# Performance work log

Measured on AMD Instinct MI355X. Metric: run time of the kernel, lower is better.

Reference implementation:

```python
import jax, jax.numpy as jnp
import numpy as np

HIDDEN = 512
ATT_DIM = 128
LN_EPS = 1e-3  # keras LayerNormalization default epsilon


def setup_inputs() -> dict:
    key = jax.random.key(0)
    k1, k2, k3, k4 = jax.random.split(key, 4)
    hidden_states = jax.random.normal(k1, (64, 2048, HIDDEN), dtype=jnp.float32)
    # Glorot-uniform style init for the dense weights
    def glorot(k, shape):
        lim = np.sqrt(6.0 / (shape[0] + shape[1]))
        return jax.random.uniform(k, shape, jnp.float32, -lim, lim)
    W_a = glorot(k2, (HIDDEN, ATT_DIM))
    U_a = glorot(k3, (HIDDEN, ATT_DIM))
    v_a = glorot(k4, (ATT_DIM, 1))
    ln_gamma = jnp.ones((HIDDEN,), jnp.float32)
    ln_beta = jnp.zeros((HIDDEN,), jnp.float32)
    return {"hidden_states": hidden_states, "W_a": W_a, "U_a": U_a,
            "v_a": v_a, "ln_gamma": ln_gamma, "ln_beta": ln_beta}


def reference(hidden_states, W_a, U_a, v_a, ln_gamma, ln_beta):
    # hidden_states: (B, L, H)
    h_att = jnp.einsum('blh,ha->bla', hidden_states, W_a)        # (B, L, A)
    context = jnp.mean(hidden_states, axis=1, keepdims=True)     # (B, 1, H)
    u_att = jnp.einsum('blh,ha->bla', context, U_a)              # (B, 1, A) broadcasts
    combined = jnp.tanh(h_att + u_att)                           # (B, L, A)
    scores = jnp.einsum('bla,ao->bl', combined, v_a)             # (B, L)
    attn = jax.nn.softmax(scores, axis=-1)                       # (B, L)
    attended = jnp.einsum('blh,bl->bh', hidden_states, attn)     # (B, H)
    # LayerNormalization over last axis
    mu = jnp.mean(attended, axis=-1, keepdims=True)
    var = jnp.var(attended, axis=-1, keepdims=True)
    normed = (attended - mu) * jax.lax.rsqrt(var + LN_EPS)
    out = normed * ln_gamma + ln_beta
    return out, attn
```

## Files before the change

kernel.cpp:

```cpp
#include <hip/hip_runtime.h>
#include <hip/hip_bf16.h>

#define HIDDEN 512
#define ATT    128
#define NB     64
#define SL     2048
#define LN_EPS 1e-3f

typedef __attribute__((ext_vector_type(8))) short short8;
typedef __attribute__((ext_vector_type(4))) float f32x4;
typedef __attribute__((ext_vector_type(2))) unsigned ux2;

__device__ __forceinline__ short f2bf(float f) {
    union { float f; unsigned u; } v; v.f = f;
    unsigned r = v.u + 0x7fffu + ((v.u >> 16) & 1u);
    return (short)(r >> 16);
}
__device__ __forceinline__ unsigned pack2bf(float lo, float hi) {
    union { __hip_bfloat162 h; unsigned u; } v;
    v.h = __float22bfloat162_rn(make_float2(lo, hi));
    return v.u;
}
__device__ __forceinline__ float bflo(unsigned u) {
    union { unsigned x; float f; } v; v.x = u << 16; return v.f;
}
__device__ __forceinline__ float bfhi(unsigned u) {
    union { unsigned x; float f; } v; v.x = u & 0xffff0000u; return v.f;
}
__device__ __forceinline__ float tanh_fast(float x) {
    float cx = fminf(fmaxf(x, -15.f), 15.f);
    float e = __expf(2.f * cx);
    return (e - 1.f) * __builtin_amdgcn_rcpf(e + 1.f);
}
__device__ __forceinline__ f32x4 nt_load4(const float* p) {
    return __builtin_nontemporal_load((const f32x4*)p);
}

__global__ void p0_wt(const float* __restrict__ W, short* __restrict__ Bp) {
    int idx = blockIdx.x * 256 + threadIdx.x;
    int j = idx & 7, lane = (idx >> 3) & 63, nt = (idx >> 9) & 7, ks = idx >> 12;
    int a = nt * 16 + (lane & 15);
    int h = ks * 32 + ((lane >> 4) << 3) + j;
    Bp[idx] = f2bf(W[h * ATT + a]);
}

__launch_bounds__(256, 3)
__global__ void p1_gemm_ctx(const float* __restrict__ hidden, const short* __restrict__ Bp,
                            short* __restrict__ h_att, float* __restrict__ ctx_part) {
    __shared__ __align__(16) short As[4][2][32 * 64];

    int t = threadIdx.x;
    int wave = t >> 6, lane = t & 63, quad = lane >> 4, cb = lane & 15;
    int row0 = blockIdx.x * 128 + wave * 32;

    f32x4 acc[2][8];
    #pragma unroll
    for (int mt = 0; mt < 2; ++mt)
        #pragma unroll
        for (int nt = 0; nt < 8; ++nt)
            acc[mt][nt] = (f32x4){0.f, 0.f, 0.f, 0.f};

    int lrow = lane >> 4;
    int col4 = lane & 15;
    const float* sbase = hidden + (size_t)(row0 + lrow) * HIDDEN + col4 * 4;
    short (*my)[32 * 64] = As[wave];
    const short8* Bp8 = (const short8*)Bp + lane;

    f32x4 g[8];

    auto issue_loads = [&](int c) {
        const float* src = sbase + c * 64;
        #pragma unroll
        for (int p = 0; p < 8; ++p)
            g[p] = nt_load4(src + (size_t)p * 4 * HIDDEN);
    };

    auto pack_write = [&](int c, int buf) {
        float s[4] = {0.f, 0.f, 0.f, 0.f};
        #pragma unroll
        for (int p = 0; p < 8; ++p) {
            int row = p * 4 + lrow;
            const f32x4 f = g[p];
            s[0] += f.x; s[1] += f.y; s[2] += f.z; s[3] += f.w;
            ux2 pk;
            pk.x = pack2bf(f.x, f.y);
            pk.y = pack2bf(f.z, f.w);
            int off = row * 64 + (((col4 >> 1) ^ (row & 7)) << 3) + ((col4 & 1) << 2);
            *(ux2*)&my[buf][off] = pk;
        }
        #pragma unroll
        for (int j = 0; j < 4; ++j) {
            s[j] += __shfl_xor(s[j], 16);
            s[j] += __shfl_xor(s[j], 32);
        }
        if (lane < 16) {
            float* cp = ctx_part + (size_t)(blockIdx.x * 4 + wave) * HIDDEN + c * 64 + lane * 4;
            __builtin_nontemporal_store((f32x4){s[0], s[1], s[2], s[3]}, (f32x4*)cp);
        }
    };

    auto compute = [&](int c, int buf) {
        int swz = cb & 7;
        #pragma unroll
        for (int s2 = 0; s2 < 2; ++s2) {
            int ks = c * 2 + s2;
            short8 b8[8];
            #pragma unroll
            for (int nt = 0; nt < 8; ++nt)
                b8[nt] = Bp8[((size_t)ks * 8 + nt) * 64];
            int blk = ((s2 * 4 + quad) ^ swz) << 3;
            short8 a0 = *(const short8*)&my[buf][cb * 64 + blk];
            short8 a1 = *(const short8*)&my[buf][(cb + 16) * 64 + blk];
            #pragma unroll
            for (int nt = 0; nt < 8; ++nt) {
                acc[0][nt] = __builtin_amdgcn_mfma_f32_16x16x32_bf16(a0, b8[nt], acc[0][nt], 0, 0, 0);
                acc[1][nt] = __builtin_amdgcn_mfma_f32_16x16x32_bf16(a1, b8[nt], acc[1][nt], 0, 0, 0);
            }
        }
    };

    issue_loads(0);
    pack_write(0, 0);
    for (int c = 0; c < 8; ++c) {
        compute(c, c & 1);
        if (c < 7) {
            issue_loads(c + 1);
            pack_write(c + 1, (c + 1) & 1);
        }
    }

    ux2* hp = (ux2*)h_att;
    size_t base = (((size_t)blockIdx.x * 4 + wave) * 2) * 8 * 64 + lane;
    #pragma unroll
    for (int mt = 0; mt < 2; ++mt)
        #pragma unroll
        for (int nt = 0; nt < 8; ++nt) {
            ux2 p;
            p.x = pack2bf(acc[mt][nt][0], acc[mt][nt][1]);
            p.y = pack2bf(acc[mt][nt][2], acc[mt][nt][3]);
            __builtin_nontemporal_store(p, &hp[base + ((size_t)mt * 8 + nt) * 64]);
        }
}

__launch_bounds__(256)
__global__ void p2_uatt(const float* __restrict__ ctx_part, const float* __restrict__ U,
                        float* __restrict__ uatt) {
    int b = blockIdx.x, t = threadIdx.x;
    __shared__ float cs[HIDDEN];
    __shared__ float ds[256];
    float s0 = 0.f, s1 = 0.f;
    #pragma unroll 8
    for (int c = 0; c < 64; ++c) {
        const float* base = ctx_part + (size_t)(b * 64 + c) * HIDDEN;
        s0 += __builtin_nontemporal_load(base + t);
        s1 += __builtin_nontemporal_load(base + t + 256);
    }
    cs[t] = s0; cs[t + 256] = s1;
    __syncthreads();
    int a = t & 127, h0 = (t >> 7) * 256;
    float d = 0.f;
    #pragma unroll 8
    for (int h = 0; h < 256; ++h) d += cs[h0 + h] * U[(size_t)(h0 + h) * ATT + a];
    ds[t] = d;
    __syncthreads();
    if (t < 128) uatt[b * ATT + t] = (ds[t] + ds[t + 128]) * (1.f / SL);
}

__launch_bounds__(256)
__global__ void p3_scores(const short* __restrict__ h_att, const float* __restrict__ v_a,
                          const float* __restrict__ uatt, float* __restrict__ scores) {
    int t = threadIdx.x, bx = blockIdx.x;
    int wave = t >> 6, lane = t & 63, quad = lane >> 4, cb = lane & 15;
    int b = bx >> 4;
    int row0 = bx * 128;

    float uv[8], vv[8];
    #pragma unroll
    for (int nt = 0; nt < 8; ++nt) {
        uv[nt] = uatt[b * ATT + nt * 16 + cb];
        vv[nt] = v_a[nt * 16 + cb];
    }

    const ux2* hp = (const ux2*)h_att;
    size_t base = (((size_t)bx * 4 + wave) * 2) * 8 * 64 + lane;

    #pragma unroll
    for (int mt = 0; mt < 2; ++mt) {
        ux2 f[8];
        #pragma unroll
        for (int nt = 0; nt < 8; ++nt)
            f[nt] = __builtin_nontemporal_load(&hp[base + ((size_t)mt * 8 + nt) * 64]);
        float r[4] = {0.f, 0.f, 0.f, 0.f};
        #pragma unroll
        for (int nt = 0; nt < 8; ++nt) {
            r[0] += vv[nt] * tanh_fast(bflo(f[nt].x) + uv[nt]);
            r[1] += vv[nt] * tanh_fast(bfhi(f[nt].x) + uv[nt]);
            r[2] += vv[nt] * tanh_fast(bflo(f[nt].y) + uv[nt]);
            r[3] += vv[nt] * tanh_fast(bfhi(f[nt].y) + uv[nt]);
        }
        #pragma unroll
        for (int j = 0; j < 4; ++j) {
            r[j] += __shfl_xor(r[j], 1);
            r[j] += __shfl_xor(r[j], 2);
            r[j] += __shfl_xor(r[j], 4);
            r[j] += __shfl_xor(r[j], 8);
        }
        if (cb == 0) {
            #pragma unroll
            for (int j = 0; j < 4; ++j)
                scores[row0 + wave * 32 + mt * 16 + quad * 4 + j] = r[j];
        }
    }
}

__launch_bounds__(256)
__global__ void p4_softmax(float* __restrict__ attn) {
    int b = blockIdx.x, t = threadIdx.x;
    float* p = attn + b * SL;
    __shared__ float red[256];
    float v[8];
    float m = -1e30f;
    #pragma unroll
    for (int i = 0; i < 8; ++i) { v[i] = p[t + i * 256]; m = fmaxf(m, v[i]); }
    red[t] = m; __syncthreads();
    for (int s = 128; s > 0; s >>= 1) { if (t < s) red[t] = fmaxf(red[t], red[t + s]); __syncthreads(); }
    m = red[0]; __syncthreads();
    float sum = 0.f;
    #pragma unroll
    for (int i = 0; i < 8; ++i) { v[i] = __expf(v[i] - m); sum += v[i]; }
    red[t] = sum; __syncthreads();
    for (int s = 128; s > 0; s >>= 1) { if (t < s) red[t] += red[t + s]; __syncthreads(); }
    float inv = 1.f / red[0];
    #pragma unroll
    for (int i = 0; i < 8; ++i) p[t + i * 256] = v[i] * inv;
}

__launch_bounds__(256)
__global__ void p5_attended(const float* __restrict__ hidden, const float* __restrict__ attn,
                            float* __restrict__ att_part) {
    int b = blockIdx.y, c = blockIdx.x, t = threadIdx.x;
    __shared__ float w_s[128];
    __shared__ f32x4 red_s[128];
    if (t < 128) w_s[t] = attn[b * SL + c * 128 + t];
    __syncthreads();
    int cg = t & 127, half = t >> 7;
    const float* hp = hidden + ((size_t)b * SL + c * 128 + half * 64) * HIDDEN + cg * 4;
    f32x4 a = {0.f, 0.f, 0.f, 0.f};
    #pragma unroll 4
    for (int l = 0; l < 64; ++l) {
        float w = w_s[half * 64 + l];
        const f32x4 g = nt_load4(hp + (size_t)l * HIDDEN);
        a.x += w * g.x; a.y += w * g.y; a.z += w * g.z; a.w += w * g.w;
    }
    if (half) red_s[cg] = a;
    __syncthreads();
    if (!half) {
        f32x4 r = red_s[cg];
        a.x += r.x; a.y += r.y; a.z += r.z; a.w += r.w;
        __builtin_nontemporal_store(a, (f32x4*)(att_part + ((size_t)(c * NB + b)) * HIDDEN + cg * 4));
    }
}

__launch_bounds__(256)
__global__ void p6_ln(const float* __restrict__ att_part, const float* __restrict__ gamma,
                      const float* __restrict__ beta, float* __restrict__ out) {
    int b = blockIdx.x, t = threadIdx.x;
    float x0 = 0.f, x1 = 0.f;
    #pragma unroll
    for (int c = 0; c < 16; ++c) {
        size_t base = (size_t)(c * NB + b) * HIDDEN;
        x0 += __builtin_nontemporal_load(att_part + base + t);
        x1 += __builtin_nontemporal_load(att_part + base + t + 256);
    }
    __shared__ float rs[256], rq[256];
    rs[t] = x0 + x1; rq[t] = x0 * x0 + x1 * x1;
    __syncthreads();
    for (int s = 128; s > 0; s >>= 1) {
        if (t < s) { rs[t] += rs[t + s]; rq[t] += rq[t + s]; }
        __syncthreads();
    }
    float mean = rs[0] * (1.f / HIDDEN);
    float var = rq[0] * (1.f / HIDDEN) - mean * mean;
    float r = rsqrtf(var + LN_EPS);
    out[b * HIDDEN + t]       = (x0 - mean) * r * gamma[t] + beta[t];
    out[b * HIDDEN + t + 256] = (x1 - mean) * r * gamma[t + 256] + beta[t + 256];
}

extern "C" void kernel_launch(void* const* d_in, const int* in_sizes, int n_in,
                              void* d_out, int out_size, void* d_ws, size_t ws_size,
                              hipStream_t stream) {
    const float* hidden = (const float*)d_in[0];
    const float* W      = (const float*)d_in[1];
    const float* U      = (const float*)d_in[2];
    const float* v_a    = (const float*)d_in[3];
    const float* gamma  = (const float*)d_in[4];
    const float* beta   = (const float*)d_in[5];

    float* out  = (float*)d_out;
    float* attn = out + NB * HIDDEN;

    short* h_att    = (short*)d_ws;
    float* ctx_part = (float*)((char*)d_ws + (size_t)NB * SL * ATT * 2);
    float* att_part = ctx_part + (size_t)4096 * HIDDEN;
    float* uatt     = att_part + (size_t)16 * NB * HIDDEN;
    short* Bp       = (short*)(uatt + NB * ATT);

    p0_wt<<<256, 256, 0, stream>>>(W, Bp);
    p1_gemm_ctx<<<(NB * SL) / 128, 256, 0, stream>>>(hidden, Bp, h_att, ctx_part);
    p2_uatt<<<NB, 256, 0, stream>>>(ctx_part, U, uatt);
    p3_scores<<<(NB * SL) / 128, 256, 0, stream>>>(h_att, v_a, uatt, attn);
    p4_softmax<<<NB, 256, 0, stream>>>(attn);
    p5_attended<<<dim3(16, NB), 256, 0, stream>>>(hidden, attn, att_part);
    p6_ln<<<NB, 256, 0, stream>>>(att_part, gamma, beta, out);
}
```

Baseline: 442.9 us.

## Stage GEMM input via direct global-to-LDS loads and reverse attended-pass order for cache reuse

The GEMM kernel now copies fp32 hidden-state tiles straight into LDS with global_load_lds, using an XOR-swizzled layout. It converts them to bf16 only when reading MFMA operands, and the context partial sums are read back from LDS. This removes the register round-trip and the separate pack/write stage, at the cost of twice the LDS footprint and occupancy lowered from 3 to 2 blocks. Nontemporal loads are replaced with regular cached loads, and the attended pass walks blocks in reverse order, presumably to hit the tail of hidden_states still resident in cache from the GEMM pass.

```diff
diff --git a/kernel.cpp b/kernel.cpp
--- a/kernel.cpp
+++ b/kernel.cpp
@@ -32,8 +32,9 @@
     float e = __expf(2.f * cx);
     return (e - 1.f) * __builtin_amdgcn_rcpf(e + 1.f);
 }
-__device__ __forceinline__ f32x4 nt_load4(const float* p) {
-    return __builtin_nontemporal_load((const f32x4*)p);
+__device__ __forceinline__ void gld_lds16(const float* g, float* lds) {
+    __builtin_amdgcn_global_load_lds((const __attribute__((address_space(1))) void*)g,
+                                     (__attribute__((address_space(3))) void*)lds, 16, 0, 0);
 }
 
 __global__ void p0_wt(const float* __restrict__ W, short* __restrict__ Bp) {
@@ -44,14 +45,14 @@
     Bp[idx] = f2bf(W[h * ATT + a]);
 }
 
-__launch_bounds__(256, 3)
+__launch_bounds__(256, 2)
 __global__ void p1_gemm_ctx(const float* __restrict__ hidden, const short* __restrict__ Bp,
                             short* __restrict__ h_att, float* __restrict__ ctx_part) {
-    __shared__ __align__(16) short As[4][2][32 * 64];
+    __shared__ __align__(16) float Asf[4][2][32 * 64];
 
     int t = threadIdx.x;
     int wave = t >> 6, lane = t & 63, quad = lane >> 4, cb = lane & 15;
-    int row0 = blockIdx.x * 128 + wave * 32;
+    int row0b = blockIdx.x * 128 + wave * 32;
 
     f32x4 acc[2][8];
     #pragma unroll
@@ -60,72 +61,79 @@
         for (int nt = 0; nt < 8; ++nt)
             acc[mt][nt] = (f32x4){0.f, 0.f, 0.f, 0.f};
 
-    int lrow = lane >> 4;
-    int col4 = lane & 15;
-    const float* sbase = hidden + (size_t)(row0 + lrow) * HIDDEN + col4 * 4;
-    short (*my)[32 * 64] = As[wave];
+    const float* gsrc[8];
+    #pragma unroll
+    for (int p = 0; p < 8; ++p) {
+        int row = p * 4 + (lane >> 4);
+        int blkp = (lane & 15) ^ (row & 15);
+        gsrc[p] = hidden + (size_t)(row0b + row) * HIDDEN + blkp * 4;
+    }
+    float (*my)[32 * 64] = Asf[wave];
     const short8* Bp8 = (const short8*)Bp + lane;
 
-    f32x4 g[8];
-
-    auto issue_loads = [&](int c) {
-        const float* src = sbase + c * 64;
+    auto stage = [&](int c, int buf) {
         #pragma unroll
         for (int p = 0; p < 8; ++p)
-            g[p] = nt_load4(src + (size_t)p * 4 * HIDDEN);
+            gld_lds16(gsrc[p] + c * 64, &my[buf][p * 256]);
     };
 
-    auto pack_write = [&](int c, int buf) {
-        float s[4] = {0.f, 0.f, 0.f, 0.f};
-        #pragma unroll
-        for (int p = 0; p < 8; ++p) {
-            int row = p * 4 + lrow;
-            const f32x4 f = g[p];
-            s[0] += f.x; s[1] += f.y; s[2] += f.z; s[3] += f.w;
-            ux2 pk;
-            pk.x = pack2bf(f.x, f.y);
-            pk.y = pack2bf(f.z, f.w);
-            int off = row * 64 + (((col4 >> 1) ^ (row & 7)) << 3) + ((col4 & 1) << 2);
-            *(ux2*)&my[buf][off] = pk;
-        }
-        #pragma unroll
-        for (int j = 0; j < 4; ++j) {
-            s[j] += __shfl_xor(s[j], 16);
-            s[j] += __shfl_xor(s[j], 32);
-        }
-        if (lane < 16) {
-            float* cp = ctx_part + (size_t)(blockIdx.x * 4 + wave) * HIDDEN + c * 64 + lane * 4;
-            __builtin_nontemporal_store((f32x4){s[0], s[1], s[2], s[3]}, (f32x4*)cp);
-        }
-    };
-
-    auto compute = [&](int c, int buf) {
-        int swz = cb & 7;
+    stage(0, 0);
+
+    for (int c = 0; c < 8; ++c) {
+        int buf = c & 1;
+
+        short8 b8[2][8];
+        #pragma unroll
+        for (int s2 = 0; s2 < 2; ++s2)
+            #pragma unroll
+            for (int nt = 0; nt < 8; ++nt)
+                b8[s2][nt] = Bp8[((size_t)(c * 2 + s2) * 8 + nt) * 64];
+        __builtin_amdgcn_sched_barrier(0);
+
+        if (c < 7) stage(c + 1, buf ^ 1);
+        __builtin_amdgcn_sched_barrier(0);
+
+        asm volatile("s_waitcnt vmcnt(8)" ::: "memory");
+        __builtin_amdgcn_sched_barrier(0);
+
         #pragma unroll
         for (int s2 = 0; s2 < 2; ++s2) {
-            int ks = c * 2 + s2;
-            short8 b8[8];
-            #pragma unroll
-            for (int nt = 0; nt < 8; ++nt)
-                b8[nt] = Bp8[((size_t)ks * 8 + nt) * 64];
-            int blk = ((s2 * 4 + quad) ^ swz) << 3;
-            short8 a0 = *(const short8*)&my[buf][cb * 64 + blk];
-            short8 a1 = *(const short8*)&my[buf][(cb + 16) * 64 + blk];
+            int lb0 = (s2 * 4 + quad) * 2;
+            int o0 = (lb0 ^ cb) * 4, o1 = ((lb0 + 1) ^ cb) * 4;
+            f32x4 a0lo = *(const f32x4*)&my[buf][cb * 64 + o0];
+            f32x4 a0hi = *(const f32x4*)&my[buf][cb * 64 + o1];
+            f32x4 a1lo = *(const f32x4*)&my[buf][(cb + 16) * 64 + o0];
+            f32x4 a1hi = *(const f32x4*)&my[buf][(cb + 16) * 64 + o1];
+            union { short8 s8; unsigned u[4]; } a0p, a1p;
+            a0p.u[0] = pack2bf(a0lo.x, a0lo.y); a0p.u[1] = pack2bf(a0lo.z, a0lo.w);
+            a0p.u[2] = pack2bf(a0hi.x, a0hi.y); a0p.u[3] = pack2bf(a0hi.z, a0hi.w);
+            a1p.u[0] = pack2bf(a1lo.x, a1lo.y); a1p.u[1] = pack2bf(a1lo.z, a1lo.w);
+            a1p.u[2] = pack2bf(a1hi.x, a1hi.y); a1p.u[3] = pack2bf(a1hi.z, a1hi.w);
             #pragma unroll
             for (int nt = 0; nt < 8; ++nt) {
-                acc[0][nt] = __builtin_amdgcn_mfma_f32_16x16x32_bf16(a0, b8[nt], acc[0][nt], 0, 0, 0);
-                acc[1][nt] = __builtin_amdgcn_mfma_f32_16x16x32_bf16(a1, b8[nt], acc[1][nt], 0, 0, 0);
+                acc[0][nt] = __builtin_amdgcn_mfma_f32_16x16x32_bf16(a0p.s8, b8[s2][nt], acc[0][nt], 0, 0, 0);
+                acc[1][nt] = __builtin_amdgcn_mfma_f32_16x16x32_bf16(a1p.s8, b8[s2][nt], acc[1][nt], 0, 0, 0);
             }
         }
-    };
-
-    issue_loads(0);
-    pack_write(0, 0);
-    for (int c = 0; c < 8; ++c) {
-        compute(c, c & 1);
-        if (c < 7) {
-            issue_loads(c + 1);
-            pack_write(c + 1, (c + 1) & 1);
+
+        {
+            float s[4] = {0.f, 0.f, 0.f, 0.f};
+            #pragma unroll
+            for (int p = 0; p < 8; ++p) {
+                int row = p * 4 + (lane >> 4);
+                int phys = ((lane & 15) ^ (row & 15)) * 4;
+                f32x4 f = *(const f32x4*)&my[buf][row * 64 + phys];
+                s[0] += f.x; s[1] += f.y; s[2] += f.z; s[3] += f.w;
+            }
+            #pragma unroll
+            for (int j = 0; j < 4; ++j) {
+                s[j] += __shfl_xor(s[j], 16);
+                s[j] += __shfl_xor(s[j], 32);
+            }
+            if (lane < 16) {
+                float* cp = ctx_part + (size_t)(blockIdx.x * 4 + wave) * HIDDEN + c * 64 + lane * 4;
+                __builtin_nontemporal_store((f32x4){s[0], s[1], s[2], s[3]}, (f32x4*)cp);
+            }
         }
     }
 
@@ -152,8 +160,8 @@
     #pragma unroll 8
     for (int c = 0; c < 64; ++c) {
         const float* base = ctx_part + (size_t)(b * 64 + c) * HIDDEN;
-        s0 += __builtin_nontemporal_load(base + t);
-        s1 += __builtin_nontemporal_load(base + t + 256);
+        s0 += base[t];
+        s1 += base[t + 256];
     }
     cs[t] = s0; cs[t + 256] = s1;
     __syncthreads();
@@ -189,7 +197,7 @@
         ux2 f[8];
         #pragma unroll
         for (int nt = 0; nt < 8; ++nt)
-            f[nt] = __builtin_nontemporal_load(&hp[base + ((size_t)mt * 8 + nt) * 64]);
+            f[nt] = hp[base + ((size_t)mt * 8 + nt) * 64];
         float r[4] = {0.f, 0.f, 0.f, 0.f};
         #pragma unroll
         for (int nt = 0; nt < 8; ++nt) {
@@ -238,7 +246,7 @@
 __launch_bounds__(256)
 __global__ void p5_attended(const float* __restrict__ hidden, const float* __restrict__ attn,
                             float* __restrict__ att_part) {
-    int b = blockIdx.y, c = blockIdx.x, t = threadIdx.x;
+    int b = (NB - 1) - blockIdx.y, c = 15 - blockIdx.x, t = threadIdx.x;
     __shared__ float w_s[128];
     __shared__ f32x4 red_s[128];
     if (t < 128) w_s[t] = attn[b * SL + c * 128 + t];
@@ -249,7 +257,7 @@
     #pragma unroll 4
     for (int l = 0; l < 64; ++l) {
         float w = w_s[half * 64 + l];
-        const f32x4 g = nt_load4(hp + (size_t)l * HIDDEN);
+        const f32x4 g = *(const f32x4*)(hp + (size_t)l * HIDDEN);
         a.x += w * g.x; a.y += w * g.y; a.z += w * g.z; a.w += w * g.w;
     }
     if (half) red_s[cg] = a;
@@ -269,8 +277,8 @@
     #pragma unroll
     for (int c = 0; c < 16; ++c) {
         size_t base = (size_t)(c * NB + b) * HIDDEN;
-        x0 += __builtin_nontemporal_load(att_part + base + t);
-        x1 += __builtin_nontemporal_load(att_part + base + t + 256);
+        x0 += att_part[base + t];
+        x1 += att_part[base + t + 256];
     }
     __shared__ float rs[256], rq[256];
     rs[t] = x0 + x1; rq[t] = x0 * x0 + x1 * x1;
```

New measurement: 455.2 us. +2.8%, slower.

## Stream GEMM A tiles via global_load_lds with 16-row waves and double buffering

Applied to the files above, without the earlier changes.

The h_att GEMM now loads fp32 hidden rows straight into LDS with the global_load_lds DMA path, double-buffered with explicit vmcnt waits. Each wave handles 16 rows instead of 32, converting to bf16 at fragment read time and summing the context partials from LDS. Downstream kernels, grid sizes and the ctx_part layout are adjusted to the finer split. The aim is to cut register-staged load/pack overhead and raise occupancy, at the cost of twice as many ctx partials and less reuse of B fragments per wave.

```diff
diff --git a/kernel.cpp b/kernel.cpp
--- a/kernel.cpp
+++ b/kernel.cpp
@@ -34,6 +34,10 @@
 }
 __device__ __forceinline__ f32x4 nt_load4(const float* p) {
     return __builtin_nontemporal_load((const f32x4*)p);
+}
+__device__ __forceinline__ void gld_lds16(const float* g, float* lds) {
+    __builtin_amdgcn_global_load_lds((const __attribute__((address_space(1))) void*)g,
+                                     (__attribute__((address_space(3))) void*)lds, 16, 0, 0);
 }
 
 __global__ void p0_wt(const float* __restrict__ W, short* __restrict__ Bp) {
@@ -44,102 +48,90 @@
     Bp[idx] = f2bf(W[h * ATT + a]);
 }
 
-__launch_bounds__(256, 3)
+__launch_bounds__(256, 4)
 __global__ void p1_gemm_ctx(const float* __restrict__ hidden, const short* __restrict__ Bp,
                             short* __restrict__ h_att, float* __restrict__ ctx_part) {
-    __shared__ __align__(16) short As[4][2][32 * 64];
+    __shared__ __align__(16) float Asf[4][2][16 * 32];
 
     int t = threadIdx.x;
     int wave = t >> 6, lane = t & 63, quad = lane >> 4, cb = lane & 15;
-    int row0 = blockIdx.x * 128 + wave * 32;
-
-    f32x4 acc[2][8];
-    #pragma unroll
-    for (int mt = 0; mt < 2; ++mt)
+    int gw = blockIdx.x * 4 + wave;
+    int row0 = gw * 16;
+
+    f32x4 acc[8];
+    #pragma unroll
+    for (int nt = 0; nt < 8; ++nt) acc[nt] = (f32x4){0.f, 0.f, 0.f, 0.f};
+
+    int lr = lane >> 3;
+    int lc = lane & 7;
+    int blkp = lc ^ lr;
+    const float* g0 = hidden + (size_t)(row0 + lr) * HIDDEN + blkp * 4;
+    float (*my)[16 * 32] = Asf[wave];
+    const short8* Bp8 = (const short8*)Bp + lane;
+
+    auto stage = [&](int c, int buf) {
+        gld_lds16(g0 + c * 32,                      &my[buf][0]);
+        gld_lds16(g0 + (size_t)8 * HIDDEN + c * 32, &my[buf][8 * 32]);
+    };
+
+    stage(0, 0);
+
+    for (int c = 0; c < 16; ++c) {
+        int buf = c & 1;
+
+        short8 b8[8];
         #pragma unroll
         for (int nt = 0; nt < 8; ++nt)
-            acc[mt][nt] = (f32x4){0.f, 0.f, 0.f, 0.f};
-
-    int lrow = lane >> 4;
-    int col4 = lane & 15;
-    const float* sbase = hidden + (size_t)(row0 + lrow) * HIDDEN + col4 * 4;
-    short (*my)[32 * 64] = As[wave];
-    const short8* Bp8 = (const short8*)Bp + lane;
-
-    f32x4 g[8];
-
-    auto issue_loads = [&](int c) {
-        const float* src = sbase + c * 64;
-        #pragma unroll
-        for (int p = 0; p < 8; ++p)
-            g[p] = nt_load4(src + (size_t)p * 4 * HIDDEN);
-    };
-
-    auto pack_write = [&](int c, int buf) {
-        float s[4] = {0.f, 0.f, 0.f, 0.f};
-        #pragma unroll
-        for (int p = 0; p < 8; ++p) {
-            int row = p * 4 + lrow;
-            const f32x4 f = g[p];
-            s[0] += f.x; s[1] += f.y; s[2] += f.z; s[3] += f.w;
-            ux2 pk;
-            pk.x = pack2bf(f.x, f.y);
-            pk.y = pack2bf(f.z, f.w);
-            int off = row * 64 + (((col4 >> 1) ^ (row & 7)) << 3) + ((col4 & 1) << 2);
-            *(ux2*)&my[buf][off] = pk;
-        }
-        #pragma unroll
-        for (int j = 0; j < 4; ++j) {
-            s[j] += __shfl_xor(s[j], 16);
-            s[j] += __shfl_xor(s[j], 32);
-        }
-        if (lane < 16) {
-            float* cp = ctx_part + (size_t)(blockIdx.x * 4 + wave) * HIDDEN + c * 64 + lane * 4;
-            __builtin_nontemporal_store((f32x4){s[0], s[1], s[2], s[3]}, (f32x4*)cp);
-        }
-    };
-
-    auto compute = [&](int c, int buf) {
-        int swz = cb & 7;
-        #pragma unroll
-        for (int s2 = 0; s2 < 2; ++s2) {
-            int ks = c * 2 + s2;
-            short8 b8[8];
+            b8[nt] = Bp8[((size_t)c * 8 + nt) * 64];
+        __builtin_amdgcn_sched_barrier(0);
+
+        if (c < 15) stage(c + 1, buf ^ 1);
+        __builtin_amdgcn_sched_barrier(0);
+
+        if (c < 15) { asm volatile("s_waitcnt vmcnt(2)" ::: "memory"); }
+        else        { asm volatile("s_waitcnt vmcnt(0)" ::: "memory"); }
+        __builtin_amdgcn_sched_barrier(0);
+
+        {
+            int lb0 = quad * 2;
+            int o0 = ((lb0 ^ (cb & 7)) << 2);
+            int o1 = (((lb0 + 1) ^ (cb & 7)) << 2);
+            f32x4 alo = *(const f32x4*)&my[buf][cb * 32 + o0];
+            f32x4 ahi = *(const f32x4*)&my[buf][cb * 32 + o1];
+            union { short8 s8; unsigned u[4]; } ap;
+            ap.u[0] = pack2bf(alo.x, alo.y); ap.u[1] = pack2bf(alo.z, alo.w);
+            ap.u[2] = pack2bf(ahi.x, ahi.y); ap.u[3] = pack2bf(ahi.z, ahi.w);
             #pragma unroll
             for (int nt = 0; nt < 8; ++nt)
-                b8[nt] = Bp8[((size_t)ks * 8 + nt) * 64];
-            int blk = ((s2 * 4 + quad) ^ swz) << 3;
-            short8 a0 = *(const short8*)&my[buf][cb * 64 + blk];
-            short8 a1 = *(const short8*)&my[buf][(cb + 16) * 64 + blk];
+                acc[nt] = __builtin_amdgcn_mfma_f32_16x16x32_bf16(ap.s8, b8[nt], acc[nt], 0, 0, 0);
+        }
+
+        {
+            f32x4 f0 = *(const f32x4*)&my[buf][lr * 32 + (blkp << 2)];
+            f32x4 f1 = *(const f32x4*)&my[buf][(lr + 8) * 32 + (blkp << 2)];
+            float s[4] = { f0.x + f1.x, f0.y + f1.y, f0.z + f1.z, f0.w + f1.w };
             #pragma unroll
-            for (int nt = 0; nt < 8; ++nt) {
-                acc[0][nt] = __builtin_amdgcn_mfma_f32_16x16x32_bf16(a0, b8[nt], acc[0][nt], 0, 0, 0);
-                acc[1][nt] = __builtin_amdgcn_mfma_f32_16x16x32_bf16(a1, b8[nt], acc[1][nt], 0, 0, 0);
+            for (int j = 0; j < 4; ++j) {
+                s[j] += __shfl_xor(s[j], 8);
+                s[j] += __shfl_xor(s[j], 16);
+                s[j] += __shfl_xor(s[j], 32);
+            }
+            if (lane < 8) {
+                float* cp = ctx_part + (size_t)gw * HIDDEN + c * 32 + lane * 4;
+                __builtin_nontemporal_store((f32x4){s[0], s[1], s[2], s[3]}, (f32x4*)cp);
             }
         }
-    };
-
-    issue_loads(0);
-    pack_write(0, 0);
-    for (int c = 0; c < 8; ++c) {
-        compute(c, c & 1);
-        if (c < 7) {
-            issue_loads(c + 1);
-            pack_write(c + 1, (c + 1) & 1);
-        }
     }
 
     ux2* hp = (ux2*)h_att;
-    size_t base = (((size_t)blockIdx.x * 4 + wave) * 2) * 8 * 64 + lane;
-    #pragma unroll
-    for (int mt = 0; mt < 2; ++mt)
-        #pragma unroll
-        for (int nt = 0; nt < 8; ++nt) {
-            ux2 p;
-            p.x = pack2bf(acc[mt][nt][0], acc[mt][nt][1]);
-            p.y = pack2bf(acc[mt][nt][2], acc[mt][nt][3]);
-            __builtin_nontemporal_store(p, &hp[base + ((size_t)mt * 8 + nt) * 64]);
-        }
+    size_t base = (size_t)gw * 8 * 64 + lane;
+    #pragma unroll
+    for (int nt = 0; nt < 8; ++nt) {
+        ux2 p;
+        p.x = pack2bf(acc[nt][0], acc[nt][1]);
+        p.y = pack2bf(acc[nt][2], acc[nt][3]);
+        __builtin_nontemporal_store(p, &hp[base + (size_t)nt * 64]);
+    }
 }
 
 __launch_bounds__(256)
@@ -150,8 +142,8 @@
     __shared__ float ds[256];
     float s0 = 0.f, s1 = 0.f;
     #pragma unroll 8
-    for (int c = 0; c < 64; ++c) {
-        const float* base = ctx_part + (size_t)(b * 64 + c) * HIDDEN;
+    for (int c = 0; c < 128; ++c) {
+        const float* base = ctx_part + (size_t)(b * 128 + c) * HIDDEN;
         s0 += __builtin_nontemporal_load(base + t);
         s1 += __builtin_nontemporal_load(base + t + 256);
     }
@@ -171,8 +163,8 @@
                           const float* __restrict__ uatt, float* __restrict__ scores) {
     int t = threadIdx.x, bx = blockIdx.x;
     int wave = t >> 6, lane = t & 63, quad = lane >> 4, cb = lane & 15;
-    int b = bx >> 4;
-    int row0 = bx * 128;
+    int gw = bx * 4 + wave;
+    int b = gw >> 7;
 
     float uv[8], vv[8];
     #pragma unroll
@@ -182,34 +174,31 @@
     }
 
     const ux2* hp = (const ux2*)h_att;
-    size_t base = (((size_t)bx * 4 + wave) * 2) * 8 * 64 + lane;
-
-    #pragma unroll
-    for (int mt = 0; mt < 2; ++mt) {
-        ux2 f[8];
+    size_t base = (size_t)gw * 8 * 64 + lane;
+
+    ux2 f[8];
+    #pragma unroll
+    for (int nt = 0; nt < 8; ++nt)
+        f[nt] = __builtin_nontemporal_load(&hp[base + (size_t)nt * 64]);
+    float r[4] = {0.f, 0.f, 0.f, 0.f};
+    #pragma unroll
+    for (int nt = 0; nt < 8; ++nt) {
+        r[0] += vv[nt] * tanh_fast(bflo(f[nt].x) + uv[nt]);
+        r[1] += vv[nt] * tanh_fast(bfhi(f[nt].x) + uv[nt]);
+        r[2] += vv[nt] * tanh_fast(bflo(f[nt].y) + uv[nt]);
+        r[3] += vv[nt] * tanh_fast(bfhi(f[nt].y) + uv[nt]);
+    }
+    #pragma unroll
+    for (int j = 0; j < 4; ++j) {
+        r[j] += __shfl_xor(r[j], 1);
+        r[j] += __shfl_xor(r[j], 2);
+        r[j] += __shfl_xor(r[j], 4);
+        r[j] += __shfl_xor(r[j], 8);
+    }
+    if (cb == 0) {
         #pragma unroll
-        for (int nt = 0; nt < 8; ++nt)
-            f[nt] = __builtin_nontemporal_load(&hp[base + ((size_t)mt * 8 + nt) * 64]);
-        float r[4] = {0.f, 0.f, 0.f, 0.f};
-        #pragma unroll
-        for (int nt = 0; nt < 8; ++nt) {
-            r[0] += vv[nt] * tanh_fast(bflo(f[nt].x) + uv[nt]);
-            r[1] += vv[nt] * tanh_fast(bfhi(f[nt].x) + uv[nt]);
-            r[2] += vv[nt] * tanh_fast(bflo(f[nt].y) + uv[nt]);
-            r[3] += vv[nt] * tanh_fast(bfhi(f[nt].y) + uv[nt]);
-        }
-        #pragma unroll
-        for (int j = 0; j < 4; ++j) {
-            r[j] += __shfl_xor(r[j], 1);
-            r[j] += __shfl_xor(r[j], 2);
-            r[j] += __shfl_xor(r[j], 4);
-            r[j] += __shfl_xor(r[j], 8);
-        }
-        if (cb == 0) {
-            #pragma unroll
-            for (int j = 0; j < 4; ++j)
-                scores[row0 + wave * 32 + mt * 16 + quad * 4 + j] = r[j];
-        }
+        for (int j = 0; j < 4; ++j)
+            scores[gw * 16 + quad * 4 + j] = r[j];
     }
 }
 
@@ -301,14 +290,14 @@
 
     short* h_att    = (short*)d_ws;
     float* ctx_part = (float*)((char*)d_ws + (size_t)NB * SL * ATT * 2);
-    float* att_part = ctx_part + (size_t)4096 * HIDDEN;
+    float* att_part = ctx_part + (size_t)8192 * HIDDEN;
     float* uatt     = att_part + (size_t)16 * NB * HIDDEN;
     short* Bp       = (short*)(uatt + NB * ATT);
 
     p0_wt<<<256, 256, 0, stream>>>(W, Bp);
-    p1_gemm_ctx<<<(NB * SL) / 128, 256, 0, stream>>>(hidden, Bp, h_att, ctx_part);
+    p1_gemm_ctx<<<(NB * SL) / 64, 256, 0, stream>>>(hidden, Bp, h_att, ctx_part);
     p2_uatt<<<NB, 256, 0, stream>>>(ctx_part, U, uatt);
-    p3_scores<<<(NB * SL) / 128, 256, 0, stream>>>(h_att, v_a, uatt, attn);
+    p3_scores<<<(NB * SL) / 64, 256, 0, stream>>>(h_att, v_a, uatt, attn);
     p4_softmax<<<NB, 256, 0, stream>>>(attn);
     p5_attended<<<dim3(16, NB), 256, 0, stream>>>(hidden, attn, att_part);
     p6_ln<<<NB, 256, 0, stream>>>(att_part, gamma, beta, out);
```

Measured after the change: 471.8 us. +6.5%, slower.
